# Optimization experiments

Measured on AMD Instinct MI355X. Metric: run time of the kernel, lower is better.

Reference implementation:

```python
import jax, jax.numpy as jnp
import numpy as np

EMBED_DIM = 1024
NUM_HEADS = 16
HEAD_DIM = EMBED_DIM // NUM_HEADS
SCALING = HEAD_DIM ** (-0.5)
BSZ, SEQ = 2, 2048


def setup_inputs() -> dict:
    key = jax.random.key(0)
    ks = jax.random.split(key, 12)
    s = 1.0 / np.sqrt(EMBED_DIM)
    query = jax.random.normal(ks[0], (BSZ, SEQ, EMBED_DIM), dtype=jnp.float32)
    return {
        "query": query,
        "key": query,
        "value": query,
        "attn_bias": jax.random.normal(ks[1], (BSZ, NUM_HEADS, SEQ, SEQ), dtype=jnp.float32) * 0.1,
        "Wq": jax.random.normal(ks[2], (EMBED_DIM, EMBED_DIM), dtype=jnp.float32) * s,
        "bq": jax.random.normal(ks[3], (EMBED_DIM,), dtype=jnp.float32) * 0.01,
        "Wk": jax.random.normal(ks[4], (EMBED_DIM, EMBED_DIM), dtype=jnp.float32) * s,
        "bk": jax.random.normal(ks[5], (EMBED_DIM,), dtype=jnp.float32) * 0.01,
        "Wv": jax.random.normal(ks[6], (EMBED_DIM, EMBED_DIM), dtype=jnp.float32) * s,
        "bv": jax.random.normal(ks[7], (EMBED_DIM,), dtype=jnp.float32) * 0.01,
        "Wo": jax.random.normal(ks[8], (EMBED_DIM, EMBED_DIM), dtype=jnp.float32) * s,
        "bo": jax.random.normal(ks[9], (EMBED_DIM,), dtype=jnp.float32) * 0.01,
    }


def reference(query, key, value, attn_bias, Wq, bq, Wk, bk, Wv, bv, Wo, bo):
    # Self-attention: k and v are computed from `query` (key/value args ignored
    # by the original module). torch Linear: y = x @ W.T + b
    B, T, E = query.shape
    H, D = NUM_HEADS, HEAD_DIM
    q = (query @ Wq.T + bq) * SCALING
    k = query @ Wk.T + bk
    v = query @ Wv.T + bv
    # [B, T, H, D]
    q = q.reshape(B, T, H, D)
    k = k.reshape(B, T, H, D)
    v = v.reshape(B, T, H, D)
    # scores: [B, H, T, T]
    scores = jnp.einsum("bthd,bshd->bhts", q, k) + attn_bias
    probs = jax.nn.softmax(scores, axis=-1)
    # attention output: [B, T, H, D] -> [B, T, E]
    attn = jnp.einsum("bhts,bshd->bthd", probs, v).reshape(B, T, E)
    out = attn @ Wo.T + bo
    # need_weights=True default: average attention weights over heads [B, T, T]
    avg_weights = probs.mean(axis=1)
    return out, avg_weights
```

## Files before the change

### kernel.cpp

```cpp
#include <hip/hip_runtime.h>
#include <hip/hip_bf16.h>

#define B_ 2
#define H_ 16
#define T_ 2048
#define D_ 64
#define ED_ 1024

typedef __attribute__((ext_vector_type(8))) short bf16x8;
typedef __attribute__((ext_vector_type(4))) float f32x4;

__device__ __forceinline__ void gload16(const void* g, void* l) {
  __builtin_amdgcn_global_load_lds(
      (const __attribute__((address_space(1))) unsigned int*)(uintptr_t)g,
      (__attribute__((address_space(3))) unsigned int*)(uintptr_t)l,
      16, 0, 0);
}

__device__ __forceinline__ float b2f(short s) {
  unsigned int u = ((unsigned int)(unsigned short)s) << 16;
  return __builtin_bit_cast(float, u);
}

__global__ __launch_bounds__(256) void convert_f32_bf16(
    const float* __restrict__ x, const float* __restrict__ wq, const float* __restrict__ wk,
    const float* __restrict__ wv, const float* __restrict__ wo,
    __hip_bfloat16* __restrict__ xb, __hip_bfloat16* __restrict__ wqb,
    __hip_bfloat16* __restrict__ wkb, __hip_bfloat16* __restrict__ wvb,
    __hip_bfloat16* __restrict__ wob)
{
  int id = blockIdx.x * 256 + threadIdx.x;
  size_t e0 = (size_t)id * 4;
  const float* src; __hip_bfloat16* dst; size_t off;
  if (e0 < 4194304) { src = x; dst = xb; off = e0; }
  else {
    size_t r = e0 - 4194304;
    int wsel = (int)(r >> 20);
    off = r & 1048575;
    src = (wsel == 0) ? wq : (wsel == 1) ? wk : (wsel == 2) ? wv : wo;
    dst = (wsel == 0) ? wqb : (wsel == 1) ? wkb : (wsel == 2) ? wvb : wob;
  }
  float4 v = *(const float4*)(src + off);
  __hip_bfloat16 o[4];
  o[0] = __float2bfloat16(v.x); o[1] = __float2bfloat16(v.y);
  o[2] = __float2bfloat16(v.z); o[3] = __float2bfloat16(v.w);
  *(ushort4*)(dst + off) = *(ushort4*)o;
}

struct GemmP {
  const __hip_bfloat16* A;
  const __hip_bfloat16* Bw[3];
  const float* bias[3];
  void* out[3];
  float scale[3];
  int mode[3];
};

__global__ __launch_bounds__(256, 2) void gemm_nt(GemmP p)
{
  __shared__ __hip_bfloat16 As[128 * 64];
  __shared__ __hip_bfloat16 Bs[128 * 64];
  const int tid = threadIdx.x;
  const int z = blockIdx.z;
  const __hip_bfloat16* A = p.A;
  const __hip_bfloat16* Bw = p.Bw[z];
  const int bm0 = blockIdx.x * 128, bn0 = blockIdx.y * 128;
  const int l = tid & 63, w = tid >> 6;
  const int wr = w >> 1, wc = w & 1;
  const int lhi = l >> 4, llo = l & 15;
  const int swl = (llo & 7) << 3;

  f32x4 acc[4][4];
#pragma unroll
  for (int m = 0; m < 4; ++m)
#pragma unroll
    for (int n = 0; n < 4; ++n) acc[m][n] = (f32x4){0.f, 0.f, 0.f, 0.f};

  for (int kt = 0; kt < 1024; kt += 64) {
#pragma unroll
    for (int j = 0; j < 4; ++j) {
      int off = j * 2048 + tid * 8;
      int row = off >> 6;
      int col = off & 63;
      int cs = col ^ ((row & 7) << 3);
      gload16(&A[(size_t)(bm0 + row) * 1024 + kt + cs], &As[off]);
      gload16(&Bw[(size_t)(bn0 + row) * 1024 + kt + cs], &Bs[off]);
    }
    __syncthreads();
#pragma unroll
    for (int kk = 0; kk < 2; ++kk) {
      bf16x8 af[4], bf[4];
#pragma unroll
      for (int m = 0; m < 4; ++m)
        af[m] = *(const bf16x8*)&As[(wr * 64 + m * 16 + llo) * 64 + ((kk * 32 + lhi * 8) ^ swl)];
#pragma unroll
      for (int n = 0; n < 4; ++n)
        bf[n] = *(const bf16x8*)&Bs[(wc * 64 + n * 16 + llo) * 64 + ((kk * 32 + lhi * 8) ^ swl)];
#pragma unroll
      for (int m = 0; m < 4; ++m)
#pragma unroll
        for (int n = 0; n < 4; ++n)
          acc[m][n] = __builtin_amdgcn_mfma_f32_16x16x32_bf16(af[m], bf[n], acc[m][n], 0, 0, 0);
    }
    __syncthreads();
  }

  const float* bias = p.bias[z];
  const float scale = p.scale[z];
  const int mode = p.mode[z];
  float bv[4];
#pragma unroll
  for (int n = 0; n < 4; ++n) bv[n] = bias[bn0 + wc * 64 + n * 16 + llo];
#pragma unroll
  for (int m = 0; m < 4; ++m) {
    int rowb = bm0 + wr * 64 + m * 16 + lhi * 4;
#pragma unroll
    for (int n = 0; n < 4; ++n) {
      int col = bn0 + wc * 64 + n * 16 + llo;
#pragma unroll
      for (int r = 0; r < 4; ++r) {
        float v = (acc[m][n][r] + bv[n]) * scale;
        int row = rowb + r;
        if (mode == 0) {
          ((__hip_bfloat16*)p.out[z])[(size_t)row * 1024 + col] = __float2bfloat16(v);
        } else if (mode == 1) {
          ((float*)p.out[z])[(size_t)row * 1024 + col] = v;
        } else {
          int bb = row >> 11, t = row & 2047;
          int hh = col >> 6, d = col & 63;
          ((__hip_bfloat16*)p.out[z])[((size_t)((bb * 16 + hh) * 64 + d)) * 2048 + t] =
              __float2bfloat16(v);
        }
      }
    }
  }
}

__global__ __launch_bounds__(256, 4) void attn_fwd(
    const __hip_bfloat16* __restrict__ qb,
    const __hip_bfloat16* __restrict__ kb,
    const __hip_bfloat16* __restrict__ vT,
    const float* __restrict__ bias,
    unsigned char* __restrict__ Ebuf,
    float* __restrict__ invl,
    __hip_bfloat16* __restrict__ attn)
{
  __shared__ __hip_bfloat16 Ks[64 * 64];
  __shared__ __hip_bfloat16 Vs[64 * 64];
  __shared__ float          bS[64 * 64];
  __shared__ __hip_bfloat16 Ps[64 * 64];
  const int tid = threadIdx.x;
  const int l = tid & 63, w = tid >> 6;
  const int lhi = l >> 4, llo = l & 15;
  const int swl = (llo & 7) << 3;
  const int qt = blockIdx.x, h = blockIdx.y, b = blockIdx.z;
  const int t0 = qt * 64;
  const __hip_bfloat16* kbase = kb + ((size_t)b * 2048) * 1024 + h * 64;
  const __hip_bfloat16* vbase = vT + ((size_t)((b * 16 + h) * 64)) * 2048;
  const float* bbase = bias + (((size_t)(b * 16 + h)) * 2048 + t0) * 2048;
  unsigned char* ebase = Ebuf + (((size_t)(b * 16 + h)) * 2048 + t0) * 2048;

  bf16x8 qa[2];
#pragma unroll
  for (int kk = 0; kk < 2; ++kk)
    qa[kk] = *(const bf16x8*)&qb[((size_t)(b * 2048 + t0 + w * 16 + llo)) * 1024 +
                                 h * 64 + kk * 32 + lhi * 8];

  f32x4 acc_o[4];
#pragma unroll
  for (int f = 0; f < 4; ++f) acc_o[f] = (f32x4){0.f, 0.f, 0.f, 0.f};
  float lrun[4] = {0.f, 0.f, 0.f, 0.f};

  const int er = tid >> 2, ec = (tid & 3) << 4;
  const int esw = (er & 7) << 3;

  for (int it = 0; it < 32; ++it) {
    const int s0 = it * 64;
#pragma unroll
    for (int j = 0; j < 2; ++j) {
      int off = j * 2048 + tid * 8;
      int row = off >> 6, col = off & 63;
      int cs = col ^ ((row & 7) << 3);
      gload16(&kbase[(size_t)(s0 + row) * 1024 + cs], &Ks[off]);
      gload16(&vbase[(size_t)row * 2048 + s0 + cs], &Vs[off]);
    }
#pragma unroll
    for (int j = 0; j < 4; ++j) {
      int off = j * 1024 + tid * 4;
      int row = off >> 6, col = off & 63;
      int cs = col ^ (((row >> 2) & 3) << 4);
      gload16(&bbase[(size_t)row * 2048 + s0 + cs], &bS[off]);
    }
    if (it > 0) {
      bf16x8 e0 = *(const bf16x8*)&Ps[er * 64 + (ec ^ esw)];
      bf16x8 e1 = *(const bf16x8*)&Ps[er * 64 + ((ec + 8) ^ esw)];
      unsigned int d4[4];
#pragma unroll
      for (int q = 0; q < 2; ++q) {
        int lo0 = __builtin_amdgcn_cvt_pk_fp8_f32(b2f(e0[4 * q]) * 0.0625f,
                                                  b2f(e0[4 * q + 1]) * 0.0625f, 0, 0);
        d4[q] = __builtin_amdgcn_cvt_pk_fp8_f32(b2f(e0[4 * q + 2]) * 0.0625f,
                                                b2f(e0[4 * q + 3]) * 0.0625f, lo0, 1);
        int lo1 = __builtin_amdgcn_cvt_pk_fp8_f32(b2f(e1[4 * q]) * 0.0625f,
                                                  b2f(e1[4 * q + 1]) * 0.0625f, 0, 0);
        d4[2 + q] = __builtin_amdgcn_cvt_pk_fp8_f32(b2f(e1[4 * q + 2]) * 0.0625f,
                                                    b2f(e1[4 * q + 3]) * 0.0625f, lo1, 1);
      }
      *(uint4*)&ebase[(size_t)er * 2048 + (s0 - 64) + ec] =
          make_uint4(d4[0], d4[1], d4[2], d4[3]);
    }
    __syncthreads();

    f32x4 sa[4];
#pragma unroll
    for (int f = 0; f < 4; ++f) sa[f] = (f32x4){0.f, 0.f, 0.f, 0.f};
#pragma unroll
    for (int kk = 0; kk < 2; ++kk) {
#pragma unroll
      for (int f = 0; f < 4; ++f) {
        bf16x8 kf = *(const bf16x8*)&Ks[(f * 16 + llo) * 64 + ((kk * 32 + lhi * 8) ^ swl)];
        sa[f] = __builtin_amdgcn_mfma_f32_16x16x32_bf16(qa[kk], kf, sa[f], 0, 0, 0);
      }
    }
    float rsum[4] = {0.f, 0.f, 0.f, 0.f};
#pragma unroll
    for (int f = 0; f < 4; ++f) {
      int col = f * 16 + llo;
#pragma unroll
      for (int r = 0; r < 4; ++r) {
        int row = w * 16 + lhi * 4 + r;
        float s = sa[f][r] + bS[row * 64 + (col ^ (lhi << 4))];
        float ev = __expf(s);
        rsum[r] += ev;
        Ps[row * 64 + (col ^ (((lhi * 4 + r) & 7) << 3))] = __float2bfloat16(ev);
      }
    }
#pragma unroll
    for (int r = 0; r < 4; ++r) {
      float v = rsum[r];
      v += __shfl_xor(v, 1); v += __shfl_xor(v, 2);
      v += __shfl_xor(v, 4); v += __shfl_xor(v, 8);
      lrun[r] += v;
    }
#pragma unroll
    for (int kk = 0; kk < 2; ++kk) {
      bf16x8 pa = *(const bf16x8*)&Ps[(w * 16 + llo) * 64 + ((kk * 32 + lhi * 8) ^ swl)];
#pragma unroll
      for (int f = 0; f < 4; ++f) {
        bf16x8 vf = *(const bf16x8*)&Vs[(f * 16 + llo) * 64 + ((kk * 32 + lhi * 8) ^ swl)];
        acc_o[f] = __builtin_amdgcn_mfma_f32_16x16x32_bf16(pa, vf, acc_o[f], 0, 0, 0);
      }
    }
    __syncthreads();
  }

  {
    bf16x8 e0 = *(const bf16x8*)&Ps[er * 64 + (ec ^ esw)];
    bf16x8 e1 = *(const bf16x8*)&Ps[er * 64 + ((ec + 8) ^ esw)];
    unsigned int d4[4];
#pragma unroll
    for (int q = 0; q < 2; ++q) {
      int lo0 = __builtin_amdgcn_cvt_pk_fp8_f32(b2f(e0[4 * q]) * 0.0625f,
                                                b2f(e0[4 * q + 1]) * 0.0625f, 0, 0);
      d4[q] = __builtin_amdgcn_cvt_pk_fp8_f32(b2f(e0[4 * q + 2]) * 0.0625f,
                                              b2f(e0[4 * q + 3]) * 0.0625f, lo0, 1);
      int lo1 = __builtin_amdgcn_cvt_pk_fp8_f32(b2f(e1[4 * q]) * 0.0625f,
                                                b2f(e1[4 * q + 1]) * 0.0625f, 0, 0);
      d4[2 + q] = __builtin_amdgcn_cvt_pk_fp8_f32(b2f(e1[4 * q + 2]) * 0.0625f,
                                                  b2f(e1[4 * q + 3]) * 0.0625f, lo1, 1);
    }
    *(uint4*)&ebase[(size_t)er * 2048 + (2048 - 64) + ec] =
        make_uint4(d4[0], d4[1], d4[2], d4[3]);
  }

  float inv[4];
#pragma unroll
  for (int r = 0; r < 4; ++r) inv[r] = 1.f / lrun[r];
#pragma unroll
  for (int f = 0; f < 4; ++f) {
    int d = f * 16 + llo;
#pragma unroll
    for (int r = 0; r < 4; ++r) {
      int t = t0 + w * 16 + lhi * 4 + r;
      attn[((size_t)(b * 2048 + t)) * 1024 + h * 64 + d] =
          __float2bfloat16(acc_o[f][r] * inv[r]);
    }
  }
  if (llo == 0) {
#pragma unroll
    for (int r = 0; r < 4; ++r)
      invl[((size_t)(b * 16 + h)) * 2048 + t0 + w * 16 + lhi * 4 + r] = inv[r];
  }
}

__global__ __launch_bounds__(256) void avgw_k(
    const unsigned char* __restrict__ Ebuf, const float* __restrict__ invl,
    float* __restrict__ outw)
{
  int c = blockIdx.x * 256 + threadIdx.x;
  int b = c >> 18;
  int rem = c & 262143;
  int t = rem >> 7;
  int s0 = (rem & 127) << 4;
  float acc[16];
#pragma unroll
  for (int i = 0; i < 16; ++i) acc[i] = 0.f;
#pragma unroll
  for (int hh = 0; hh < 16; ++hh) {
    float inv = invl[((size_t)(b * 16 + hh)) * 2048 + t];
    uint4 evv = *(const uint4*)&Ebuf[(((size_t)(b * 16 + hh)) * 2048 + t) * 2048 + s0];
    unsigned int dw[4] = {evv.x, evv.y, evv.z, evv.w};
#pragma unroll
    for (int q = 0; q < 4; ++q) {
      acc[q * 4 + 0] += __builtin_amdgcn_cvt_f32_fp8(dw[q], 0) * inv;
      acc[q * 4 + 1] += __builtin_amdgcn_cvt_f32_fp8(dw[q], 1) * inv;
      acc[q * 4 + 2] += __builtin_amdgcn_cvt_f32_fp8(dw[q], 2) * inv;
      acc[q * 4 + 3] += __builtin_amdgcn_cvt_f32_fp8(dw[q], 3) * inv;
    }
  }
  float* o = outw + ((size_t)(b * 2048 + t)) * 2048 + s0;
#pragma unroll
  for (int q = 0; q < 4; ++q)
    *(float4*)(o + q * 4) = make_float4(acc[q * 4], acc[q * 4 + 1], acc[q * 4 + 2], acc[q * 4 + 3]);
}

extern "C" void kernel_launch(void* const* d_in, const int* in_sizes, int n_in,
                              void* d_out, int out_size, void* d_ws, size_t ws_size,
                              hipStream_t stream) {
  const float* query     = (const float*)d_in[0];
  const float* attn_bias = (const float*)d_in[3];
  const float* Wq = (const float*)d_in[4];
  const float* bq = (const float*)d_in[5];
  const float* Wk = (const float*)d_in[6];
  const float* bk = (const float*)d_in[7];
  const float* Wv = (const float*)d_in[8];
  const float* bv = (const float*)d_in[9];
  const float* Wo = (const float*)d_in[10];
  const float* bo = (const float*)d_in[11];
  float* out = (float*)d_out;

  char* ws = (char*)d_ws;
  __hip_bfloat16* xb   = (__hip_bfloat16*)(ws + 0);
  __hip_bfloat16* wqb  = (__hip_bfloat16*)(ws + 8388608);
  __hip_bfloat16* wkb  = (__hip_bfloat16*)(ws + 10485760);
  __hip_bfloat16* wvb  = (__hip_bfloat16*)(ws + 12582912);
  __hip_bfloat16* wob  = (__hip_bfloat16*)(ws + 14680064);
  __hip_bfloat16* qbf  = (__hip_bfloat16*)(ws + 16777216);
  __hip_bfloat16* kbf  = (__hip_bfloat16*)(ws + 25165824);
  __hip_bfloat16* vTb  = (__hip_bfloat16*)(ws + 33554432);
  __hip_bfloat16* atnb = (__hip_bfloat16*)(ws + 41943040);
  float*          linv = (float*)(ws + 50331648);
  unsigned char*  Ebuf = (unsigned char*)(ws + 50593792);

  convert_f32_bf16<<<8192, 256, 0, stream>>>(query, Wq, Wk, Wv, Wo, xb, wqb, wkb, wvb, wob);

  GemmP gp{};
  gp.A = xb;
  gp.Bw[0] = wqb; gp.Bw[1] = wkb; gp.Bw[2] = wvb;
  gp.bias[0] = bq; gp.bias[1] = bk; gp.bias[2] = bv;
  gp.out[0] = qbf; gp.out[1] = kbf; gp.out[2] = vTb;
  gp.scale[0] = 0.125f; gp.scale[1] = 1.f; gp.scale[2] = 1.f;
  gp.mode[0] = 0; gp.mode[1] = 0; gp.mode[2] = 2;
  gemm_nt<<<dim3(32, 8, 3), 256, 0, stream>>>(gp);

  attn_fwd<<<dim3(32, 16, 2), 256, 0, stream>>>(qbf, kbf, vTb, attn_bias, Ebuf, linv, atnb);

  avgw_k<<<2048, 256, 0, stream>>>(Ebuf, linv, out + 4194304);

  GemmP go{};
  go.A = atnb;
  go.Bw[0] = wob; go.bias[0] = bo; go.out[0] = out;
  go.scale[0] = 1.f; go.mode[0] = 1;
  gemm_nt<<<dim3(32, 8, 1), 256, 0, stream>>>(go);
}
```

Baseline: 297.2 us.

## Load K, V and bias directly into registers and drop block-wide barriers

Removes the shared-memory staging of K, V and the bias tile. Each wave now loads its MFMA operands and bias values straight from global memory into registers. The fp8 E-buffer write is moved into the same iteration and done per-wave on the wave's own rows, so the __syncthreads barriers go away. The aim is to cut LDS traffic and barrier stalls and let waves run independently. The cost is that the four waves each reload the same K/V fragments from global memory or cache, with uncoalesced 16-byte loads and higher register pressure.

```diff
diff --git a/kernel.cpp b/kernel.cpp
--- a/kernel.cpp
+++ b/kernel.cpp
@@ -145,9 +145,6 @@
     float* __restrict__ invl,
     __hip_bfloat16* __restrict__ attn)
 {
-  __shared__ __hip_bfloat16 Ks[64 * 64];
-  __shared__ __hip_bfloat16 Vs[64 * 64];
-  __shared__ float          bS[64 * 64];
   __shared__ __hip_bfloat16 Ps[64 * 64];
   const int tid = threadIdx.x;
   const int l = tid & 63, w = tid >> 6;
@@ -171,29 +168,61 @@
   for (int f = 0; f < 4; ++f) acc_o[f] = (f32x4){0.f, 0.f, 0.f, 0.f};
   float lrun[4] = {0.f, 0.f, 0.f, 0.f};
 
-  const int er = tid >> 2, ec = (tid & 3) << 4;
-  const int esw = (er & 7) << 3;
+  const int erl = w * 16 + (l >> 2), ec = (l & 3) << 4;
+  const int esw = (erl & 7) << 3;
 
   for (int it = 0; it < 32; ++it) {
     const int s0 = it * 64;
-#pragma unroll
-    for (int j = 0; j < 2; ++j) {
-      int off = j * 2048 + tid * 8;
-      int row = off >> 6, col = off & 63;
-      int cs = col ^ ((row & 7) << 3);
-      gload16(&kbase[(size_t)(s0 + row) * 1024 + cs], &Ks[off]);
-      gload16(&vbase[(size_t)row * 2048 + s0 + cs], &Vs[off]);
-    }
-#pragma unroll
-    for (int j = 0; j < 4; ++j) {
-      int off = j * 1024 + tid * 4;
-      int row = off >> 6, col = off & 63;
-      int cs = col ^ (((row >> 2) & 3) << 4);
-      gload16(&bbase[(size_t)row * 2048 + s0 + cs], &bS[off]);
-    }
-    if (it > 0) {
-      bf16x8 e0 = *(const bf16x8*)&Ps[er * 64 + (ec ^ esw)];
-      bf16x8 e1 = *(const bf16x8*)&Ps[er * 64 + ((ec + 8) ^ esw)];
+    float bb[4][4];
+#pragma unroll
+    for (int f = 0; f < 4; ++f)
+#pragma unroll
+      for (int r = 0; r < 4; ++r)
+        bb[f][r] = bbase[(size_t)(w * 16 + lhi * 4 + r) * 2048 + s0 + f * 16 + llo];
+    bf16x8 kf[2][4];
+#pragma unroll
+    for (int kk = 0; kk < 2; ++kk)
+#pragma unroll
+      for (int f = 0; f < 4; ++f)
+        kf[kk][f] = *(const bf16x8*)&kbase[(size_t)(s0 + f * 16 + llo) * 1024 +
+                                           kk * 32 + lhi * 8];
+    f32x4 sa[4];
+#pragma unroll
+    for (int f = 0; f < 4; ++f) sa[f] = (f32x4){0.f, 0.f, 0.f, 0.f};
+#pragma unroll
+    for (int kk = 0; kk < 2; ++kk)
+#pragma unroll
+      for (int f = 0; f < 4; ++f)
+        sa[f] = __builtin_amdgcn_mfma_f32_16x16x32_bf16(qa[kk], kf[kk][f], sa[f], 0, 0, 0);
+    bf16x8 vf[2][4];
+#pragma unroll
+    for (int kk = 0; kk < 2; ++kk)
+#pragma unroll
+      for (int f = 0; f < 4; ++f)
+        vf[kk][f] = *(const bf16x8*)&vbase[(size_t)(f * 16 + llo) * 2048 +
+                                           s0 + kk * 32 + lhi * 8];
+    float rsum[4] = {0.f, 0.f, 0.f, 0.f};
+#pragma unroll
+    for (int f = 0; f < 4; ++f) {
+      int col = f * 16 + llo;
+#pragma unroll
+      for (int r = 0; r < 4; ++r) {
+        int row = w * 16 + lhi * 4 + r;
+        float ev = __expf(sa[f][r] + bb[f][r]);
+        rsum[r] += ev;
+        Ps[row * 64 + (col ^ (((lhi * 4 + r) & 7) << 3))] = __float2bfloat16(ev);
+      }
+    }
+#pragma unroll
+    for (int r = 0; r < 4; ++r) {
+      float v = rsum[r];
+      v += __shfl_xor(v, 1); v += __shfl_xor(v, 2);
+      v += __shfl_xor(v, 4); v += __shfl_xor(v, 8);
+      lrun[r] += v;
+    }
+    {
+      bf16x8 e0 = *(const bf16x8*)&Ps[erl * 64 + (ec ^ esw)];
+      bf16x8 e1 = *(const bf16x8*)&Ps[erl * 64 + ((ec + 8) ^ esw)];
       unsigned int d4[4];
 #pragma unroll
       for (int q = 0; q < 2; ++q) {
@@ -206,71 +235,15 @@
         d4[2 + q] = __builtin_amdgcn_cvt_pk_fp8_f32(b2f(e1[4 * q + 2]) * 0.0625f,
                                                     b2f(e1[4 * q + 3]) * 0.0625f, lo1, 1);
       }
-      *(uint4*)&ebase[(size_t)er * 2048 + (s0 - 64) + ec] =
-          make_uint4(d4[0], d4[1], d4[2], d4[3]);
-    }
-    __syncthreads();
-
-    f32x4 sa[4];
-#pragma unroll
-    for (int f = 0; f < 4; ++f) sa[f] = (f32x4){0.f, 0.f, 0.f, 0.f};
-#pragma unroll
-    for (int kk = 0; kk < 2; ++kk) {
-#pragma unroll
-      for (int f = 0; f < 4; ++f) {
-        bf16x8 kf = *(const bf16x8*)&Ks[(f * 16 + llo) * 64 + ((kk * 32 + lhi * 8) ^ swl)];
-        sa[f] = __builtin_amdgcn_mfma_f32_16x16x32_bf16(qa[kk], kf, sa[f], 0, 0, 0);
-      }
-    }
-    float rsum[4] = {0.f, 0.f, 0.f, 0.f};
-#pragma unroll
-    for (int f = 0; f < 4; ++f) {
-      int col = f * 16 + llo;
-#pragma unroll
-      for (int r = 0; r < 4; ++r) {
-        int row = w * 16 + lhi * 4 + r;
-        float s = sa[f][r] + bS[row * 64 + (col ^ (lhi << 4))];
-        float ev = __expf(s);
-        rsum[r] += ev;
-        Ps[row * 64 + (col ^ (((lhi * 4 + r) & 7) << 3))] = __float2bfloat16(ev);
-      }
-    }
-#pragma unroll
-    for (int r = 0; r < 4; ++r) {
-      float v = rsum[r];
-      v += __shfl_xor(v, 1); v += __shfl_xor(v, 2);
-      v += __shfl_xor(v, 4); v += __shfl_xor(v, 8);
-      lrun[r] += v;
+      *(uint4*)&ebase[(size_t)erl * 2048 + s0 + ec] = make_uint4(d4[0], d4[1], d4[2], d4[3]);
     }
 #pragma unroll
     for (int kk = 0; kk < 2; ++kk) {
       bf16x8 pa = *(const bf16x8*)&Ps[(w * 16 + llo) * 64 + ((kk * 32 + lhi * 8) ^ swl)];
 #pragma unroll
-      for (int f = 0; f < 4; ++f) {
-        bf16x8 vf = *(const bf16x8*)&Vs[(f * 16 + llo) * 64 + ((kk * 32 + lhi * 8) ^ swl)];
-        acc_o[f] = __builtin_amdgcn_mfma_f32_16x16x32_bf16(pa, vf, acc_o[f], 0, 0, 0);
-      }
-    }
-    __syncthreads();
-  }
-
-  {
-    bf16x8 e0 = *(const bf16x8*)&Ps[er * 64 + (ec ^ esw)];
-    bf16x8 e1 = *(const bf16x8*)&Ps[er * 64 + ((ec + 8) ^ esw)];
-    unsigned int d4[4];
-#pragma unroll
-    for (int q = 0; q < 2; ++q) {
-      int lo0 = __builtin_amdgcn_cvt_pk_fp8_f32(b2f(e0[4 * q]) * 0.0625f,
-                                                b2f(e0[4 * q + 1]) * 0.0625f, 0, 0);
-      d4[q] = __builtin_amdgcn_cvt_pk_fp8_f32(b2f(e0[4 * q + 2]) * 0.0625f,
-                                              b2f(e0[4 * q + 3]) * 0.0625f, lo0, 1);
-      int lo1 = __builtin_amdgcn_cvt_pk_fp8_f32(b2f(e1[4 * q]) * 0.0625f,
-                                                b2f(e1[4 * q + 1]) * 0.0625f, 0, 0);
-      d4[2 + q] = __builtin_amdgcn_cvt_pk_fp8_f32(b2f(e1[4 * q + 2]) * 0.0625f,
-                                                  b2f(e1[4 * q + 3]) * 0.0625f, lo1, 1);
-    }
-    *(uint4*)&ebase[(size_t)er * 2048 + (2048 - 64) + ec] =
-        make_uint4(d4[0], d4[1], d4[2], d4[3]);
+      for (int f = 0; f < 4; ++f)
+        acc_o[f] = __builtin_amdgcn_mfma_f32_16x16x32_bf16(pa, vf[kk][f], acc_o[f], 0, 0, 0);
+    }
   }
 
   float inv[4];
```

Result: slower. 476.1 us (+60.2%).
